# Kernel tuning notes

Hardware: AMD Instinct MI355X
Metric: run time of the kernel (lower is better)

## Reference

```python
import jax, jax.numpy as jnp
import numpy as np

NUM_HEADS = 32
NUM_KV_HEADS = 8
HEAD_DIM = 128
SLIDING_WINDOW = 1024
ROPE_THETA = 10000.0


def _rotate_half(x):
    x1, x2 = jnp.split(x, 2, axis=-1)
    return jnp.concatenate((-x2, x1), axis=-1)


def _rope_cos_sin(seq_len, head_dim, theta, dtype):
    inv_freq = 1.0 / (theta ** (jnp.arange(0, head_dim, 2, dtype=jnp.float32) / head_dim))
    t = jnp.arange(seq_len, dtype=jnp.float32)
    freqs = t[:, None] * inv_freq[None, :]            # [S, hd/2]
    emb = jnp.concatenate((freqs, freqs), axis=-1)     # [S, hd]
    return jnp.cos(emb).astype(dtype), jnp.sin(emb).astype(dtype)


def setup_inputs() -> dict:
    key = jax.random.key(0)
    ks = jax.random.split(key, 5)
    B, S, H = 2, 2048, 4096
    kv_dim = NUM_KV_HEADS * HEAD_DIM
    scale = 1.0 / np.sqrt(H)
    return {
        "hidden_states": jax.random.normal(ks[0], (B, S, H), dtype=jnp.float32),
        "Wq": jax.random.normal(ks[1], (H, H), dtype=jnp.float32) * scale,
        "Wk": jax.random.normal(ks[2], (H, kv_dim), dtype=jnp.float32) * scale,
        "Wv": jax.random.normal(ks[3], (H, kv_dim), dtype=jnp.float32) * scale,
        "Wo": jax.random.normal(ks[4], (H, H), dtype=jnp.float32) * scale,
    }


def reference(hidden_states, Wq, Wk, Wv, Wo):
    B, S, H = hidden_states.shape
    groups = NUM_HEADS // NUM_KV_HEADS

    q = (hidden_states @ Wq).reshape(B, S, NUM_HEADS, HEAD_DIM).transpose(0, 2, 1, 3)
    k = (hidden_states @ Wk).reshape(B, S, NUM_KV_HEADS, HEAD_DIM).transpose(0, 2, 1, 3)
    v = (hidden_states @ Wv).reshape(B, S, NUM_KV_HEADS, HEAD_DIM).transpose(0, 2, 1, 3)

    cos, sin = _rope_cos_sin(S, HEAD_DIM, ROPE_THETA, q.dtype)  # [S, hd]
    q = q * cos + _rotate_half(q) * sin
    k = k * cos + _rotate_half(k) * sin

    # GQA: repeat_interleave kv heads to match query heads
    k = jnp.repeat(k, groups, axis=1)
    v = jnp.repeat(v, groups, axis=1)

    scores = jnp.einsum("bhqd,bhkd->bhqk", q, k) / np.sqrt(HEAD_DIM)

    i = jnp.arange(S)[:, None]
    j = jnp.arange(S)[None, :]
    allowed = (j <= i) & (i - j <= SLIDING_WINDOW // 2)  # causal + sliding window
    scores = jnp.where(allowed[None, None], scores, jnp.float32(-1e30))

    probs = jax.nn.softmax(scores, axis=-1)
    out = jnp.einsum("bhqk,bhkd->bhqd", probs, v)        # [B, nH, S, hd]
    out = out.transpose(0, 2, 1, 3).reshape(B, S, NUM_HEADS * HEAD_DIM)
    return out @ Wo
```

## Files before the change

kernel.cpp:

```cpp
#include <hip/hip_runtime.h>
#include <hip/hip_bf16.h>
#include <math.h>

#define BB 2
#define SS 2048
#define HH 4096
#define NH 32
#define NKV 8
#define HD 128
#define KVD (NKV*HD)
#define WIN 512
#define MROWS (BB*SS)

#define DT_BF16 1
#define DT_F32  2

typedef __hip_bfloat16 bf16;
typedef __attribute__((ext_vector_type(8))) short short8;
typedef __attribute__((ext_vector_type(4))) float f32x4;

__device__ __forceinline__ float ldf(const bf16* p){ return __bfloat162float(*p); }
__device__ __forceinline__ float ldf(const float* p){ return *p; }
__device__ __forceinline__ void stf(bf16* p, float v){ *p = __float2bfloat16(v); }
__device__ __forceinline__ void stf(float* p, float v){ *p = v; }

__global__ void detect_kernel(const void* __restrict__ w, int* __restrict__ flag)
{
  __shared__ int big;
  if (threadIdx.x == 0) big = 0;
  __syncthreads();
  const unsigned short* u = (const unsigned short*)w;
  for (int i = threadIdx.x; i < 2048; i += 256) {
    int ex = (u[i] >> 7) & 0xFF;
    if (ex >= 160) big = 1;
  }
  __syncthreads();
  if (threadIdx.x == 0) *flag = big ? DT_F32 : DT_BF16;
}

__global__ __launch_bounds__(256)
void cvt_x(const int* __restrict__ flag, const float* __restrict__ X,
           bf16* __restrict__ Y)
{
  if (*flag != DT_F32) return;
  const size_t idx = (size_t)blockIdx.x*256 + threadIdx.x;
  const f32x4 a = *(const f32x4*)(X + idx*8);
  const f32x4 b = *(const f32x4*)(X + idx*8 + 4);
  union { short8 s; bf16 h[8]; } u;
  #pragma unroll
  for (int j = 0; j < 4; j++) {
    u.h[j]     = __float2bfloat16(a[j]);
    u.h[j + 4] = __float2bfloat16(b[j]);
  }
  *(short8*)(Y + idx*8) = u.s;
}

template<typename TS>
__global__ __launch_bounds__(256)
void transpose_cvt(const int* __restrict__ flag, int mydt,
                   const TS* __restrict__ W0, const TS* __restrict__ W1,
                   bf16* __restrict__ D0, bf16* __restrict__ D1, int Kd, int Nd)
{
  if (*flag != mydt) return;
  const TS* W  = blockIdx.z ? W1 : W0;
  bf16*    WT  = blockIdx.z ? D1 : D0;
  __shared__ float tile[32][33];
  const int n0 = blockIdx.x*32, k0 = blockIdx.y*32;
  const int tx = threadIdx.x & 31, ty = threadIdx.x >> 5;
  #pragma unroll
  for (int j = 0; j < 4; j++)
    tile[ty + j*8][tx] = ldf(W + (size_t)(k0 + ty + j*8)*Nd + n0 + tx);
  __syncthreads();
  #pragma unroll
  for (int j = 0; j < 4; j++)
    WT[(size_t)(n0 + ty + j*8)*Kd + k0 + tx] = __float2bfloat16(tile[tx][ty + j*8]);
}

#define MFMA16(a,b,c) __builtin_amdgcn_mfma_f32_16x16x32_bf16(a,b,c,0,0,0)

template<typename TC>
__global__ __launch_bounds__(512)
void gemm256(const int* __restrict__ flag, int mydt,
             const bf16* __restrict__ A, const bf16* __restrict__ Bm,
             TC* __restrict__ C, int M, int N, int K)
{
  if (*flag != mydt) return;
  __shared__ __align__(16) bf16 lds[65536];
  const int tid = threadIdx.x;
  const int w = tid >> 6, lane = tid & 63;
  const int wm = w >> 2, wn = w & 3;
  const int fr = lane & 15, fq = lane >> 4;

  const int gx = gridDim.x;
  int wg = blockIdx.y*gx + blockIdx.x;
  const int cpx = (gx*gridDim.y) >> 3;
  wg = (wg & 7)*cpx + (wg >> 3);
  const int tM = (wg / gx)*256, tN = (wg % gx)*256;

  const int NT = K >> 6;

  auto stage = [&](int tt, int s){
    const int dbuf = tt & 1;
    const int hf = s & 1;
    const bf16* src = (s < 2) ? A : Bm;
    const int brow = ((s < 2) ? tM : tN) + hf*128;
    const int cbase = ((s < 2) ? 0 : 4096) + (dbuf*2 + hf)*1024;
    #pragma unroll
    for (int g = 0; g < 2; g++) {
      const int Ch = g*512 + tid;
      const int r = Ch >> 3, c = Ch & 7;
      const int cs = c ^ (r & 7);
      const bf16* gp = src + (size_t)(brow + r)*K + tt*64 + cs*8;
      char* lp = (char*)lds + (size_t)(cbase + g*512 + w*64)*16;
      __builtin_amdgcn_global_load_lds((const __attribute__((address_space(1))) void*)gp,
                                       (__attribute__((address_space(3))) void*)lp, 16, 0, 0);
    }
  };
  auto rdA = [&](int dbuf, int m, int kk) -> short8 {
    const int r = m*16 + fr;
    const int chunk = (dbuf*2 + wm)*1024 + r*8 + ((kk*4 + fq) ^ (r & 7));
    return *(const short8*)((char*)lds + (size_t)chunk*16);
  };
  auto rdB = [&](int dbuf, int n, int kk) -> short8 {
    const int rg = wn*64 + n*16 + fr;
    const int hf = rg >> 7, rr = rg & 127;
    const int chunk = 4096 + (dbuf*2 + hf)*1024 + rr*8 + ((kk*4 + fq) ^ (rr & 7));
    return *(const short8*)((char*)lds + (size_t)chunk*16);
  };

  f32x4 acc[8][4] = {};

  #pragma unroll
  for (int s = 0; s < 4; s++) stage(0, s);
  stage(1, 0); stage(1, 1);
  asm volatile("s_waitcnt vmcnt(4)" ::: "memory");
  __builtin_amdgcn_s_barrier();

  short8 a0[4][2], a1[4][2], b0[2][2], b1[2][2];
  for (int kt = 0; kt < NT; kt++) {
    const int db = kt & 1;
    #pragma unroll
    for (int m = 0; m < 4; m++){ a0[m][0]=rdA(db,m,0); a0[m][1]=rdA(db,m,1); }
    #pragma unroll
    for (int n = 0; n < 2; n++){ b0[n][0]=rdB(db,n,0); b0[n][1]=rdB(db,n,1); }
    if (kt+1 < NT) stage(kt+1, 2);
    asm volatile("s_waitcnt lgkmcnt(8)" ::: "memory");
    __builtin_amdgcn_s_barrier();
    asm volatile("s_waitcnt lgkmcnt(0)" ::: "memory");
    __builtin_amdgcn_sched_barrier(0);
    __builtin_amdgcn_s_setprio(1);
    #pragma unroll
    for (int m = 0; m < 4; m++)
      #pragma unroll
      for (int n = 0; n < 2; n++){
        acc[m][n] = MFMA16(a0[m][0], b0[n][0], acc[m][n]);
        acc[m][n] = MFMA16(a0[m][1], b0[n][1], acc[m][n]);
      }
    __builtin_amdgcn_s_setprio(0);
    __builtin_amdgcn_s_barrier();
    #pragma unroll
    for (int m = 0; m < 4; m++){ a1[m][0]=rdA(db,m+4,0); a1[m][1]=rdA(db,m+4,1); }
    #pragma unroll
    for (int n = 0; n < 2; n++){ b1[n][0]=rdB(db,n+2,0); b1[n][1]=rdB(db,n+2,1); }
    if (kt+1 < NT) stage(kt+1, 3);
    asm volatile("s_waitcnt lgkmcnt(8)" ::: "memory");
    __builtin_amdgcn_s_barrier();
    asm volatile("s_waitcnt lgkmcnt(0)" ::: "memory");
    __builtin_amdgcn_sched_barrier(0);
    __builtin_amdgcn_s_setprio(1);
    #pragma unroll
    for (int m = 0; m < 4; m++)
      #pragma unroll
      for (int n = 0; n < 2; n++){
        acc[m+4][n+2] = MFMA16(a1[m][0], b1[n][0], acc[m+4][n+2]);
        acc[m+4][n+2] = MFMA16(a1[m][1], b1[n][1], acc[m+4][n+2]);
      }
    __builtin_amdgcn_s_setprio(0);
    __builtin_amdgcn_s_barrier();
    if (kt+2 < NT) stage(kt+2, 0);
    __builtin_amdgcn_s_barrier();
    __builtin_amdgcn_s_setprio(1);
    #pragma unroll
    for (int m = 0; m < 4; m++)
      #pragma unroll
      for (int n = 0; n < 2; n++){
        acc[m][n+2] = MFMA16(a0[m][0], b1[n][0], acc[m][n+2]);
        acc[m][n+2] = MFMA16(a0[m][1], b1[n][1], acc[m][n+2]);
      }
    __builtin_amdgcn_s_setprio(0);
    __builtin_amdgcn_s_barrier();
    if (kt+2 < NT) stage(kt+2, 1);
    __builtin_amdgcn_s_barrier();
    __builtin_amdgcn_s_setprio(1);
    #pragma unroll
    for (int m = 0; m < 4; m++)
      #pragma unroll
      for (int n = 0; n < 2; n++){
        acc[m+4][n] = MFMA16(a1[m][0], b0[n][0], acc[m+4][n]);
        acc[m+4][n] = MFMA16(a1[m][1], b0[n][1], acc[m+4][n]);
      }
    __builtin_amdgcn_s_setprio(0);
    if (kt+2 < NT) { asm volatile("s_waitcnt vmcnt(4)" ::: "memory"); }
    else           { asm volatile("s_waitcnt vmcnt(0)" ::: "memory"); }
    __builtin_amdgcn_s_barrier();
  }

  #pragma unroll
  for (int m = 0; m < 8; m++)
    #pragma unroll
    for (int n = 0; n < 4; n++)
      #pragma unroll
      for (int r = 0; r < 4; r++)
        stf(C + (size_t)(tM + wm*128 + m*16 + fq*4 + r)*N + (tN + wn*64 + n*16 + fr),
            acc[m][n][r]);
}

__global__ __launch_bounds__(256)
void gemm_kv(const int* __restrict__ flag, int mydt, const bf16* __restrict__ A,
             const bf16* __restrict__ WTk, const bf16* __restrict__ WTv,
             bf16* __restrict__ Kout, bf16* __restrict__ VTout, int M, int N, int K)
{
  if (*flag != mydt) return;
  const bool vpath = blockIdx.z != 0;
  const bf16* Bm = vpath ? WTv : WTk;
  __shared__ __align__(16) bf16 As[128*32];
  __shared__ __align__(16) bf16 Bs[128*32];
  const int tid  = threadIdx.x;
  const int w    = tid >> 6;
  const int lane = tid & 63;
  const int wr = w >> 1, wc = w & 1;
  const int tM = blockIdx.y*128, tN = blockIdx.x*128;
  const int srow = tid >> 2;
  const int scol = (tid & 3) * 8;
  const int fr = lane & 15;
  const int kq = (lane >> 4) * 8;

  f32x4 acc[4][4] = {};

  for (int k0 = 0; k0 < K; k0 += 32) {
    __syncthreads();
    #pragma unroll
    for (int q = 0; q < 2; q++) {
      const int row = q*64 + srow;
      const bf16* ga = A  + (size_t)(tM + row)*K + k0 + scol;
      const bf16* gb = Bm + (size_t)(tN + row)*K + k0 + scol;
      char* la = (char*)As + q*4096 + w*1024;
      char* lb = (char*)Bs + q*4096 + w*1024;
      __builtin_amdgcn_global_load_lds((const __attribute__((address_space(1))) void*)ga,
                                       (__attribute__((address_space(3))) void*)la, 16, 0, 0);
      __builtin_amdgcn_global_load_lds((const __attribute__((address_space(1))) void*)gb,
                                       (__attribute__((address_space(3))) void*)lb, 16, 0, 0);
    }
    __syncthreads();

    short8 af[4], bfr[4];
    #pragma unroll
    for (int m = 0; m < 4; m++) af[m]  = *(const short8*)&As[(wr*64 + m*16 + fr)*32 + kq];
    #pragma unroll
    for (int n = 0; n < 4; n++) bfr[n] = *(const short8*)&Bs[(wc*64 + n*16 + fr)*32 + kq];
    #pragma unroll
    for (int m = 0; m < 4; m++)
      #pragma unroll
      for (int n = 0; n < 4; n++)
        acc[m][n] = MFMA16(af[m], bfr[n], acc[m][n]);
  }

  const int fq = lane >> 4;
  #pragma unroll
  for (int m = 0; m < 4; m++)
    #pragma unroll
    for (int n = 0; n < 4; n++)
      #pragma unroll
      for (int r = 0; r < 4; r++) {
        const int gm = tM + wr*64 + m*16 + fq*4 + r;
        const int gn = tN + wc*64 + n*16 + fr;
        if (vpath) {
          size_t idx = ((size_t)((gm >> 11)*NKV + (gn >> 7)))*((size_t)HD*SS)
                     + (size_t)(gn & 127)*SS + (gm & 2047);
          stf(VTout + idx, acc[m][n][r]);
        } else {
          stf(Kout + (size_t)gm*N + gn, acc[m][n][r]);
        }
      }
}

__global__ void rope_kernel(bf16* __restrict__ X, int nh)
{
  int idx = blockIdx.x*blockDim.x + threadIdx.x;
  int total = MROWS * nh * 64;
  if (idx >= total) return;
  int f   = idx & 63;
  int h   = (idx >> 6) % nh;
  int row = (idx >> 6) / nh;
  int s   = row & (SS - 1);
  float ang = (float)s * exp2f((float)f * -0.20762050593046014f);
  float sv, cv;
  __sincosf(ang, &sv, &cv);
  size_t base = (size_t)row*nh*HD + (size_t)h*HD;
  float x1 = ldf(X + base + f), x2 = ldf(X + base + 64 + f);
  stf(X + base + f,      x1*cv - x2*sv);
  stf(X + base + 64 + f, x2*cv + x1*sv);
}

__global__ __launch_bounds__(256, 2)
void attn_mfma(const bf16* __restrict__ Q, const bf16* __restrict__ K,
               const bf16* __restrict__ VT, bf16* __restrict__ Aout)
{
  const int i0 = blockIdx.x * 64;
  const int h  = blockIdx.y;
  const int b  = blockIdx.z;
  const int kh = h >> 2;
  const int tid = threadIdx.x;
  const int w = tid >> 6, lane = tid & 63;
  const int fr = lane & 15, fq = lane >> 4;

  __shared__ __align__(16) bf16 Qs[64*128];
  __shared__ __align__(16) bf16 Ks[64*128];
  __shared__ __align__(16) bf16 Vs[128*64];
  __shared__ __align__(16) bf16 Ps[4][16*64];

  {
    const bf16* gq = Q + (size_t)(b*SS + i0)*HH + h*HD;
    #pragma unroll
    for (int it = 0; it < 4; it++) {
      int slot = tid + it*256;
      int r = slot >> 4, cg = slot & 15;
      short8 v = *(const short8*)(gq + (size_t)r*HH + cg*8);
      *(short8*)((char*)Qs + r*256 + ((cg*16) ^ ((r & 7) << 4))) = v;
    }
  }
  __syncthreads();

  short8 qf[4];
  {
    const int qrow = w*16 + fr;
    #pragma unroll
    for (int kk = 0; kk < 4; kk++)
      qf[kk] = *(const short8*)((char*)Qs + qrow*256 + ((kk*64 + fq*16) ^ ((qrow & 7) << 4)));
  }

  const float scale = 0.08838834764831845f;
  f32x4 o[8];
  #pragma unroll
  for (int nn = 0; nn < 8; nn++) o[nn] = (f32x4){0.f, 0.f, 0.f, 0.f};
  float m_run[4] = {-1e30f, -1e30f, -1e30f, -1e30f};
  float l_run[4] = {0.f, 0.f, 0.f, 0.f};

  const int j0_lo = (i0 >= WIN) ? (i0 - WIN) : 0;

  for (int j0 = j0_lo; j0 <= i0; j0 += 64) {
    __syncthreads();
    {
      const bf16* gk = K + (size_t)(b*SS + j0)*KVD + kh*HD;
      #pragma unroll
      for (int it = 0; it < 4; it++) {
        int slot = tid + it*256;
        int r = slot >> 4, cg = slot & 15;
        short8 v = *(const short8*)(gk + (size_t)r*KVD + cg*8);
        *(short8*)((char*)Ks + r*256 + ((cg*16) ^ ((r & 7) << 4))) = v;
      }
    }
    {
      const bf16* gv = VT + ((size_t)(b*NKV + kh)*HD)*SS + j0;
      #pragma unroll
      for (int it = 0; it < 4; it++) {
        int slot = tid + it*256;
        int d = slot >> 3, jg = slot & 7;
        short8 v = *(const short8*)(gv + (size_t)d*SS + jg*8);
        *(short8*)((char*)Vs + d*128 + ((jg*16) ^ ((d & 7) << 4))) = v;
      }
    }
    __syncthreads();

    f32x4 sv[4];
    #pragma unroll
    for (int jf = 0; jf < 4; jf++) sv[jf] = (f32x4){0.f, 0.f, 0.f, 0.f};
    #pragma unroll
    for (int kk = 0; kk < 4; kk++) {
      #pragma unroll
      for (int jf = 0; jf < 4; jf++) {
        const int krow = jf*16 + fr;
        short8 kf = *(const short8*)((char*)Ks + krow*256 + ((kk*64 + fq*16) ^ ((krow & 7) << 4)));
        sv[jf] = MFMA16(qf[kk], kf, sv[jf]);
      }
    }

    const bool needmask = !((j0 >= i0 - 448) && (j0 <= i0 - 64));
    #pragma unroll
    for (int jf = 0; jf < 4; jf++)
      #pragma unroll
      for (int r = 0; r < 4; r++) {
        float x = sv[jf][r] * scale;
        if (needmask) {
          int iq = i0 + w*16 + fq*4 + r;
          int jv = j0 + jf*16 + fr;
          if (jv > iq || iq - jv > WIN) x = -1e30f;
        }
        sv[jf][r] = x;
      }

    float fac[4];
    #pragma unroll
    for (int r = 0; r < 4; r++) {
      float t = fmaxf(fmaxf(sv[0][r], sv[1][r]), fmaxf(sv[2][r], sv[3][r]));
      t = fmaxf(t, __shfl_xor(t, 1));
      t = fmaxf(t, __shfl_xor(t, 2));
      t = fmaxf(t, __shfl_xor(t, 4));
      t = fmaxf(t, __shfl_xor(t, 8));
      float mn = fmaxf(m_run[r], t);
      fac[r] = __expf(m_run[r] - mn);
      m_run[r] = mn;
    }
    #pragma unroll
    for (int r = 0; r < 4; r++) {
      float sum = 0.f;
      #pragma unroll
      for (int jf = 0; jf < 4; jf++) {
        float p = __expf(sv[jf][r] - m_run[r]);
        sv[jf][r] = p;
        sum += p;
      }
      sum += __shfl_xor(sum, 1);
      sum += __shfl_xor(sum, 2);
      sum += __shfl_xor(sum, 4);
      sum += __shfl_xor(sum, 8);
      l_run[r] = l_run[r]*fac[r] + sum;
    }

    char* pbase = (char*)(&Ps[w][0]);
    #pragma unroll
    for (int jf = 0; jf < 4; jf++)
      #pragma unroll
      for (int r = 0; r < 4; r++) {
        int q = fq*4 + r, j = jf*16 + fr;
        *(bf16*)(pbase + q*128 + ((j*2) ^ ((q & 7) << 4))) = __float2bfloat16(sv[jf][r]);
      }

    #pragma unroll
    for (int nn = 0; nn < 8; nn++)
      #pragma unroll
      for (int r = 0; r < 4; r++) o[nn][r] *= fac[r];

    #pragma unroll
    for (int kt = 0; kt < 2; kt++) {
      short8 ap = *(const short8*)(pbase + fr*128 + ((kt*64 + fq*16) ^ ((fr & 7) << 4)));
      #pragma unroll
      for (int nn = 0; nn < 8; nn++) {
        const int d = nn*16 + fr;
        short8 vf = *(const short8*)((char*)Vs + d*128 + ((kt*64 + fq*16) ^ ((d & 7) << 4)));
        o[nn] = MFMA16(ap, vf, o[nn]);
      }
    }
  }

  float inv[4];
  #pragma unroll
  for (int r = 0; r < 4; r++) inv[r] = 1.0f / l_run[r];
  bf16* ao = Aout + (size_t)(b*SS + i0 + w*16)*HH + h*HD;
  #pragma unroll
  for (int nn = 0; nn < 8; nn++)
    #pragma unroll
    for (int r = 0; r < 4; r++)
      stf(ao + (size_t)(fq*4 + r)*HH + nn*16 + fr, o[nn][r] * inv[r]);
}

extern "C" void kernel_launch(void* const* d_in, const int* in_sizes, int n_in,
                              void* d_out, int out_size, void* d_ws, size_t ws_size,
                              hipStream_t stream)
{
  char* ws = (char*)d_ws;
  const size_t MB = (size_t)1 << 20;
  int*  flag = (int*)ws;
  bf16* Q  = (bf16*)(ws + 256);
  bf16* K  = (bf16*)(ws + 256 + 32*MB);
  bf16* VT = (bf16*)(ws + 256 + 40*MB);
  bf16* S  = (bf16*)(ws + 256 + 48*MB);
  bf16* WTk = S;
  bf16* WTv = S + (size_t)KVD*HH;
  bf16* WTo = Q;
  bf16* Xb = (bf16*)d_out;

  detect_kernel<<<1, 256, 0, stream>>>(d_in[1], flag);
  cvt_x<<<MROWS*HH/8/256, 256, 0, stream>>>(flag, (const float*)d_in[0], Xb);

  auto tr1 = [&](const void* W, int Kd, int Nd, bf16* dst){
    dim3 g(Nd/32, Kd/32, 1);
    transpose_cvt<bf16 ><<<g,256,0,stream>>>(flag, DT_BF16, (const bf16 *)W, (const bf16 *)W, dst, dst, Kd, Nd);
    transpose_cvt<float><<<g,256,0,stream>>>(flag, DT_F32 , (const float*)W, (const float*)W, dst, dst, Kd, Nd);
  };

  tr1(d_in[1], HH, HH, S);
  {
    dim3 g(HH/256, MROWS/256);
    gemm256<bf16><<<g,512,0,stream>>>(flag, DT_BF16, (const bf16*)d_in[0], S, Q, MROWS, HH, HH);
    gemm256<bf16><<<g,512,0,stream>>>(flag, DT_F32 , Xb,                   S, Q, MROWS, HH, HH);
  }
  {
    dim3 gt(KVD/32, HH/32, 2);
    transpose_cvt<bf16 ><<<gt,256,0,stream>>>(flag, DT_BF16, (const bf16 *)d_in[2], (const bf16 *)d_in[3], WTk, WTv, HH, KVD);
    transpose_cvt<float><<<gt,256,0,stream>>>(flag, DT_F32 , (const float*)d_in[2], (const float*)d_in[3], WTk, WTv, HH, KVD);
    dim3 g(KVD/128, MROWS/128, 2);
    gemm_kv<<<g,256,0,stream>>>(flag, DT_BF16, (const bf16*)d_in[0], WTk, WTv, K, VT, MROWS, KVD, HH);
    gemm_kv<<<g,256,0,stream>>>(flag, DT_F32 , Xb,                   WTk, WTv, K, VT, MROWS, KVD, HH);
  }

  rope_kernel<<<(MROWS*NH *64 + 255)/256, 256, 0, stream>>>(Q, NH);
  rope_kernel<<<(MROWS*NKV*64 + 255)/256, 256, 0, stream>>>(K, NKV);
  attn_mfma<<<dim3(SS/64, NH, BB), 256, 0, stream>>>(Q, K, VT, S);

  tr1(d_in[4], HH, HH, WTo);
  {
    dim3 g(HH/256, MROWS/256);
    gemm256<bf16 ><<<g,512,0,stream>>>(flag, DT_BF16, S, WTo, (bf16 *)d_out, MROWS, HH, HH);
    gemm256<float><<<g,512,0,stream>>>(flag, DT_F32 , S, WTo, (float*)d_out, MROWS, HH, HH);
  }
}
```

Baseline: 734.5 us.

## Load attention operands directly from global, remap blocks, drop GEMM barriers

The attention kernel stops staging Q, K and V through shared memory and instead has each lane read its MFMA fragments straight from global memory. Blocks are remapped so neighbouring blocks share KV heads, and launch bounds are raised to allow more resident blocks. Separately, the GEMM main loop loses several workgroup barriers around its LDS staging, which cuts synchronization but risks read/write races on the double-buffered tiles. Removing the block-level syncs lowers LDS traffic but makes each of the four waves issue its own uncoalesced global reads, which repeats K/V fetches across waves.

After: 873.8 us. 1.19x slower.

```diff
diff --git a/kernel.cpp b/kernel.cpp
--- a/kernel.cpp
+++ b/kernel.cpp
@@ -144,8 +144,6 @@
     #pragma unroll
     for (int n = 0; n < 2; n++){ b0[n][0]=rdB(db,n,0); b0[n][1]=rdB(db,n,1); }
     if (kt+1 < NT) stage(kt+1, 2);
-    asm volatile("s_waitcnt lgkmcnt(8)" ::: "memory");
-    __builtin_amdgcn_s_barrier();
     asm volatile("s_waitcnt lgkmcnt(0)" ::: "memory");
     __builtin_amdgcn_sched_barrier(0);
     __builtin_amdgcn_s_setprio(1);
@@ -163,8 +161,6 @@
     #pragma unroll
     for (int n = 0; n < 2; n++){ b1[n][0]=rdB(db,n+2,0); b1[n][1]=rdB(db,n+2,1); }
     if (kt+1 < NT) stage(kt+1, 3);
-    asm volatile("s_waitcnt lgkmcnt(8)" ::: "memory");
-    __builtin_amdgcn_s_barrier();
     asm volatile("s_waitcnt lgkmcnt(0)" ::: "memory");
     __builtin_amdgcn_sched_barrier(0);
     __builtin_amdgcn_s_setprio(1);
@@ -178,7 +174,6 @@
     __builtin_amdgcn_s_setprio(0);
     __builtin_amdgcn_s_barrier();
     if (kt+2 < NT) stage(kt+2, 0);
-    __builtin_amdgcn_s_barrier();
     __builtin_amdgcn_s_setprio(1);
     #pragma unroll
     for (int m = 0; m < 4; m++)
@@ -190,7 +185,6 @@
     __builtin_amdgcn_s_setprio(0);
     __builtin_amdgcn_s_barrier();
     if (kt+2 < NT) stage(kt+2, 1);
-    __builtin_amdgcn_s_barrier();
     __builtin_amdgcn_s_setprio(1);
     #pragma unroll
     for (int m = 0; m < 4; m++)
@@ -302,42 +296,27 @@
   stf(X + base + 64 + f, x2*cv + x1*sv);
 }
 
-__global__ __launch_bounds__(256, 2)
+__global__ __launch_bounds__(256, 4)
 void attn_mfma(const bf16* __restrict__ Q, const bf16* __restrict__ K,
                const bf16* __restrict__ VT, bf16* __restrict__ Aout)
 {
-  const int i0 = blockIdx.x * 64;
-  const int h  = blockIdx.y;
-  const int b  = blockIdx.z;
+  int flat = (blockIdx.z*NH + blockIdx.y)*(SS/64) + blockIdx.x;
+  flat = (flat & 7)*(BB*NH*(SS/64)/8) + (flat >> 3);
+  const int i0 = (flat & 31) * 64;
+  const int h  = (flat >> 5) & 31;
+  const int b  = flat >> 10;
   const int kh = h >> 2;
   const int tid = threadIdx.x;
   const int w = tid >> 6, lane = tid & 63;
   const int fr = lane & 15, fq = lane >> 4;
 
-  __shared__ __align__(16) bf16 Qs[64*128];
-  __shared__ __align__(16) bf16 Ks[64*128];
-  __shared__ __align__(16) bf16 Vs[128*64];
   __shared__ __align__(16) bf16 Ps[4][16*64];
 
-  {
-    const bf16* gq = Q + (size_t)(b*SS + i0)*HH + h*HD;
-    #pragma unroll
-    for (int it = 0; it < 4; it++) {
-      int slot = tid + it*256;
-      int r = slot >> 4, cg = slot & 15;
-      short8 v = *(const short8*)(gq + (size_t)r*HH + cg*8);
-      *(short8*)((char*)Qs + r*256 + ((cg*16) ^ ((r & 7) << 4))) = v;
-    }
-  }
-  __syncthreads();
-
+  const int qrow = w*16 + fr;
+  const bf16* gq = Q + (size_t)(b*SS + i0 + qrow)*HH + h*HD + fq*8;
   short8 qf[4];
-  {
-    const int qrow = w*16 + fr;
-    #pragma unroll
-    for (int kk = 0; kk < 4; kk++)
-      qf[kk] = *(const short8*)((char*)Qs + qrow*256 + ((kk*64 + fq*16) ^ ((qrow & 7) << 4)));
-  }
+  #pragma unroll
+  for (int kk = 0; kk < 4; kk++) qf[kk] = *(const short8*)(gq + kk*32);
 
   const float scale = 0.08838834764831845f;
   f32x4 o[8];
@@ -349,38 +328,16 @@
   const int j0_lo = (i0 >= WIN) ? (i0 - WIN) : 0;
 
   for (int j0 = j0_lo; j0 <= i0; j0 += 64) {
-    __syncthreads();
-    {
-      const bf16* gk = K + (size_t)(b*SS + j0)*KVD + kh*HD;
-      #pragma unroll
-      for (int it = 0; it < 4; it++) {
-        int slot = tid + it*256;
-        int r = slot >> 4, cg = slot & 15;
-        short8 v = *(const short8*)(gk + (size_t)r*KVD + cg*8);
-        *(short8*)((char*)Ks + r*256 + ((cg*16) ^ ((r & 7) << 4))) = v;
-      }
-    }
-    {
-      const bf16* gv = VT + ((size_t)(b*NKV + kh)*HD)*SS + j0;
-      #pragma unroll
-      for (int it = 0; it < 4; it++) {
-        int slot = tid + it*256;
-        int d = slot >> 3, jg = slot & 7;
-        short8 v = *(const short8*)(gv + (size_t)d*SS + jg*8);
-        *(short8*)((char*)Vs + d*128 + ((jg*16) ^ ((d & 7) << 4))) = v;
-      }
-    }
-    __syncthreads();
-
+    const bf16* gk = K + (size_t)(b*SS + j0)*KVD + kh*HD + fq*8;
     f32x4 sv[4];
     #pragma unroll
     for (int jf = 0; jf < 4; jf++) sv[jf] = (f32x4){0.f, 0.f, 0.f, 0.f};
     #pragma unroll
-    for (int kk = 0; kk < 4; kk++) {
-      #pragma unroll
-      for (int jf = 0; jf < 4; jf++) {
-        const int krow = jf*16 + fr;
-        short8 kf = *(const short8*)((char*)Ks + krow*256 + ((kk*64 + fq*16) ^ ((krow & 7) << 4)));
+    for (int jf = 0; jf < 4; jf++) {
+      const bf16* gkr = gk + (size_t)(jf*16 + fr)*KVD;
+      #pragma unroll
+      for (int kk = 0; kk < 4; kk++) {
+        short8 kf = *(const short8*)(gkr + kk*32);
         sv[jf] = MFMA16(qf[kk], kf, sv[jf]);
       }
     }
@@ -441,13 +398,14 @@
       #pragma unroll
       for (int r = 0; r < 4; r++) o[nn][r] *= fac[r];
 
+    const bf16* gv = VT + ((size_t)(b*NKV + kh)*HD)*SS + j0 + fq*8;
     #pragma unroll
     for (int kt = 0; kt < 2; kt++) {
       short8 ap = *(const short8*)(pbase + fr*128 + ((kt*64 + fq*16) ^ ((fr & 7) << 4)));
       #pragma unroll
       for (int nn = 0; nn < 8; nn++) {
         const int d = nn*16 + fr;
-        short8 vf = *(const short8*)((char*)Vs + d*128 + ((kt*64 + fq*16) ^ ((d & 7) << 4)));
+        short8 vf = *(const short8*)(gv + (size_t)d*SS + kt*32);
         o[nn] = MFMA16(ap, vf, o[nn]);
       }
     }
```
